# Kernel optimization log

Hardware: AMD Instinct MI355X
Metric: run time of the kernel (lower is better)

## Reference

```python
import jax, jax.numpy as jnp
import numpy as np

N, D0, D1, D2 = 8192, 512, 256, 64


def setup_inputs() -> dict:
    key = jax.random.key(0)
    k1, k2, k3, k4 = jax.random.split(key, 4)
    xi = jax.random.normal(k1, (N, D0), dtype=jnp.float32)
    # graph filter ~ row-normalized adjacency: nonnegative, entries O(1/N)
    filter_matrix = jax.random.uniform(k2, (N, N), dtype=jnp.float32) * (2.0 / N)
    b1 = np.sqrt(6.0 / (D0 + D1))
    b2 = np.sqrt(6.0 / (D1 + D2))
    w1 = jax.random.uniform(k3, (D0, D1), dtype=jnp.float32, minval=-b1, maxval=b1)
    w2 = jax.random.uniform(k4, (D1, D2), dtype=jnp.float32, minval=-b2, maxval=b2)
    return {"xi": xi, "filter_matrix": filter_matrix, "w1": w1, "w2": w2}


def reference(xi, filter_matrix, w1, w2):
    # two GCN layers: F @ (X @ W)
    h = jax.nn.relu(filter_matrix @ (xi @ w1))          # [N, D1]
    emb = filter_matrix @ (h @ w2)                       # [N, D2]
    # pairwise squared Euclidean distances between rows of emb -> [N, N]
    sq = jnp.sum(emb * emb, axis=1)                      # [N]
    dists = jnp.maximum(sq[:, None] + sq[None, :] - 2.0 * (emb @ emb.T), 0.0)
    recons_w = jax.nn.softmax(-dists, axis=1)            # row softmax of negative distances
    return emb, recons_w + 1e-10
```

## Files before the change

kernel.cpp:

```cpp
#include <hip/hip_runtime.h>

typedef short s16x8 __attribute__((ext_vector_type(8)));
typedef float f32x4 __attribute__((ext_vector_type(4)));
typedef unsigned int u32;

#define DEV static __device__ __forceinline__

DEV unsigned short f2bf(float x){
  u32 u = __builtin_bit_cast(u32, x);
  return (unsigned short)((u + 0x7FFFu + ((u >> 16) & 1u)) >> 16);
}
DEV float bf2f(unsigned short h){ u32 u = ((u32)h) << 16; return __builtin_bit_cast(float, u); }
DEV u32 pack2(float a, float b){ return (u32)f2bf(a) | ((u32)f2bf(b) << 16); }

DEV void gld16(const void* g, void* l){
  __builtin_amdgcn_global_load_lds((const __attribute__((address_space(1))) u32*)g,
                                   (__attribute__((address_space(3))) u32*)l, 16, 0, 0);
}

__global__ void k_cvt(const float* __restrict__ src, unsigned short* __restrict__ dst, long n4){
  long i = (long)blockIdx.x*256 + threadIdx.x;
  long stride = (long)gridDim.x*256;
  for (; i < n4; i += stride){
    float4 v = ((const float4*)src)[i];
    int2 p; p.x = (int)pack2(v.x, v.y); p.y = (int)pack2(v.z, v.w);
    ((int2*)dst)[i] = p;
  }
}

__global__ void k_transpose_bf16(const float* __restrict__ src,
                                 unsigned short* __restrict__ dst, int R, int C){
  int idx = blockIdx.x * 256 + threadIdx.x;
  if (idx >= R * C) return;
  int r = idx / C, c = idx % C;
  dst[(size_t)c * R + r] = f2bf(src[idx]);
}

__global__ void k_relu_bf16(const float* __restrict__ src, unsigned short* __restrict__ dst, int n4){
  int idx = blockIdx.x*256 + threadIdx.x;
  if (idx >= n4) return;
  float4 v = ((const float4*)src)[idx];
  int2 p;
  p.x = (int)pack2(fmaxf(v.x,0.f), fmaxf(v.y,0.f));
  p.y = (int)pack2(fmaxf(v.z,0.f), fmaxf(v.w,0.f));
  ((int2*)dst)[idx] = p;
}

template<int ROWS,int BK,int THREADS>
DEV void stage_lds(const unsigned short* __restrict__ src, int row0, int ld,
                   int kk, char* lds, int tid){
  constexpr int SLOTS = BK/8, SLM = SLOTS-1, RPC = 64/SLOTS;
  constexpr int NCH = ROWS*BK*2/1024;
  constexpr int NW = THREADS/64, NI = NCH/NW;
  static_assert(NI*NW==NCH, "chunk exact");
  const int lane = tid & 63, wid = tid >> 6;
  #pragma unroll
  for (int i=0;i<NI;i++){
    int c = i*NW + wid;
    int r = c*RPC + lane/SLOTS;
    int s = lane & SLM;
    int ks = s ^ (r & SLM);
    gld16(src + (size_t)(row0+r)*ld + kk + ks*8, lds + c*1024);
  }
}

template<int BM,int BN,int BK,int WR,int WC,bool ATOMIC>
__global__ __launch_bounds__(WR*WC*64)
void k_gemm(const unsigned short* __restrict__ A, const unsigned short* __restrict__ B,
            void* __restrict__ Cp, int lda, int ldb, int ldc, int kchunk)
{
  constexpr int THREADS = WR*WC*64;
  constexpr int ROWB = BK*2, SLM = BK/8 - 1;
  constexpr int ABYTES = BM*ROWB, BBYTES = BN*ROWB;
  constexpr int WM = BM/WR, WN = BN/WC;
  constexpr int FM = WM/16, FN = WN/16, KS = BK/32;

  __shared__ char smem[2*(ABYTES+BBYTES)];
  char* A0 = smem; char* B0 = A0 + ABYTES;
  char* A1 = B0 + BBYTES; char* B1 = A1 + ABYTES;

  const int tid = threadIdx.x, lane = tid & 63;
  const int wid = tid >> 6, wrr = wid / WC, wcc = wid % WC;
  const int m0 = blockIdx.y * BM, n0 = blockIdx.x * BN;
  const int kbeg = blockIdx.z * kchunk, nk = kchunk / BK;

  f32x4 acc[FM][FN];
  f32x4 z4 = {0.f,0.f,0.f,0.f};
  #pragma unroll
  for (int m=0;m<FM;m++)
    #pragma unroll
    for (int n=0;n<FN;n++) acc[m][n] = z4;

  auto issue = [&](int kk, char* bA, char* bB){
    stage_lds<BM,BK,THREADS>(A, m0, lda, kk, bA, tid);
    stage_lds<BN,BK,THREADS>(B, n0, ldb, kk, bB, tid);
  };
  auto compute = [&](const char* bA, const char* bB){
    #pragma unroll
    for (int ks=0;ks<KS;ks++){
      s16x8 av[FM], bv[FN];
      #pragma unroll
      for (int m=0;m<FM;m++){
        int r = wrr*WM + m*16 + (lane&15);
        int s = (ks*4 + (lane>>4)) ^ (r & SLM);
        av[m] = *(const s16x8*)(bA + r*ROWB + s*16);
      }
      #pragma unroll
      for (int n=0;n<FN;n++){
        int r = wcc*WN + n*16 + (lane&15);
        int s = (ks*4 + (lane>>4)) ^ (r & SLM);
        bv[n] = *(const s16x8*)(bB + r*ROWB + s*16);
      }
      #pragma unroll
      for (int m=0;m<FM;m++)
        #pragma unroll
        for (int n=0;n<FN;n++)
          acc[m][n] = __builtin_amdgcn_mfma_f32_16x16x32_bf16(av[m], bv[n], acc[m][n], 0, 0, 0);
    }
  };

  issue(kbeg, A0, B0);
  __syncthreads();

  for (int t=0;t<nk;t++){
    char* cA = (t&1)?A1:A0; char* cB = (t&1)?B1:B0;
    char* nA = (t&1)?A0:A1; char* nB = (t&1)?B0:B1;
    if (t+1 < nk) issue(kbeg + (t+1)*BK, nA, nB);
    compute(cA, cB);
    __syncthreads();
  }

  if constexpr (ATOMIC) {
    float* Cf = (float*)Cp;
    #pragma unroll
    for (int m=0;m<FM;m++)
      #pragma unroll
      for (int n=0;n<FN;n++)
        #pragma unroll
        for (int r=0;r<4;r++){
          int row = m0 + wrr*WM + m*16 + (lane>>4)*4 + r;
          int col = n0 + wcc*WN + n*16 + (lane&15);
          atomicAdd(Cf + (size_t)row*ldc + col, acc[m][n][r]);
        }
  } else {
    unsigned short* Ch = (unsigned short*)Cp;
    #pragma unroll
    for (int m=0;m<FM;m++)
      #pragma unroll
      for (int n=0;n<FN;n++)
        #pragma unroll
        for (int r=0;r<4;r++){
          int row = m0 + wrr*WM + m*16 + (lane>>4)*4 + r;
          int col = n0 + wcc*WN + n*16 + (lane&15);
          Ch[(size_t)row*ldc + col] = f2bf(acc[m][n][r]);
        }
  }
}

__global__ void k_emb_fin(const float* __restrict__ acc, float* __restrict__ emb_out,
                          unsigned short* __restrict__ embb, float* __restrict__ sq){
  int idx = blockIdx.x*256 + threadIdx.x;
  float v = acc[idx];
  emb_out[idx] = v;
  unsigned short ub = f2bf(v);
  embb[idx] = ub;
  float x = bf2f(ub);
  float s = x*x;
  #pragma unroll
  for (int off=32; off>0; off>>=1) s += __shfl_xor(s, off, 64);
  if ((threadIdx.x & 63)==0) sq[idx>>6] = s;
}

template<int PASS>
__global__ __launch_bounds__(256)
void k_dist(const unsigned short* __restrict__ embb, const float* __restrict__ sq,
            float* __restrict__ S, float* __restrict__ out)
{
  constexpr int ROWB = 128, SLM = 7;
  __shared__ char smem[2*128*128];
  char* bufA = smem;
  char* bufB = smem + 128*ROWB;
  const int tid=threadIdx.x, lane=tid&63, wid=tid>>6;
  const int wrr = wid>>1, wcc = wid&1;
  const int i0 = blockIdx.y*128, j0 = blockIdx.x*128;

  #pragma unroll
  for (int i=0;i<4;i++){
    int u = tid + i*256;
    int r = u>>3, c = u&7;
    int byte = r*ROWB + ((c^(r&SLM))*16);
    *(int4*)(bufA+byte) = *(const int4*)(embb + (size_t)(i0+r)*64 + c*8);
    *(int4*)(bufB+byte) = *(const int4*)(embb + (size_t)(j0+r)*64 + c*8);
  }
  __syncthreads();

  f32x4 acc[4][4];
  f32x4 z4 = {0.f,0.f,0.f,0.f};
  #pragma unroll
  for (int m=0;m<4;m++)
    #pragma unroll
    for (int n=0;n<4;n++) acc[m][n]=z4;

  #pragma unroll
  for (int ks=0;ks<2;ks++){
    s16x8 av[4], bv[4];
    #pragma unroll
    for (int m=0;m<4;m++){
      int r = wrr*64 + m*16 + (lane&15);
      int slot = (ks*4 + (lane>>4)) ^ (r&SLM);
      av[m] = *(const s16x8*)(bufA + r*ROWB + slot*16);
    }
    #pragma unroll
    for (int n=0;n<4;n++){
      int r = wcc*64 + n*16 + (lane&15);
      int slot = (ks*4 + (lane>>4)) ^ (r&SLM);
      bv[n] = *(const s16x8*)(bufB + r*ROWB + slot*16);
    }
    #pragma unroll
    for (int m=0;m<4;m++)
      #pragma unroll
      for (int n=0;n<4;n++)
        acc[m][n] = __builtin_amdgcn_mfma_f32_16x16x32_bf16(av[m], bv[n], acc[m][n], 0, 0, 0);
  }

  float sqj[4];
  #pragma unroll
  for (int n=0;n<4;n++) sqj[n] = sq[j0 + wcc*64 + n*16 + (lane&15)];

  #pragma unroll
  for (int m=0;m<4;m++){
    #pragma unroll
    for (int r=0;r<4;r++){
      int row = i0 + wrr*64 + m*16 + (lane>>4)*4 + r;
      float sqi = sq[row];
      if constexpr (PASS==1){
        float v = 0.f;
        #pragma unroll
        for (int n=0;n<4;n++){
          float d = fmaxf(sqi + sqj[n] - 2.f*acc[m][n][r], 0.f);
          v += __expf(-d);
        }
        #pragma unroll
        for (int off=1; off<16; off<<=1) v += __shfl_xor(v, off, 64);
        if ((lane&15)==0) atomicAdd(S+row, v);
      } else {
        float inv = 1.0f / S[row];
        #pragma unroll
        for (int n=0;n<4;n++){
          int col = j0 + wcc*64 + n*16 + (lane&15);
          float d = fmaxf(sqi + sqj[n] - 2.f*acc[m][n][r], 0.f);
          out[(size_t)row*8192 + col] = __expf(-d)*inv + 1e-10f;
        }
      }
    }
  }
}

extern "C" void kernel_launch(void* const* d_in, const int* in_sizes, int n_in,
                              void* d_out, int out_size, void* d_ws, size_t ws_size,
                              hipStream_t stream)
{
  const float* xi = (const float*)d_in[0];
  const float* F  = (const float*)d_in[1];
  const float* w1 = (const float*)d_in[2];
  const float* w2 = (const float*)d_in[3];
  float* out = (float*)d_out;
  float* emb_out = out;
  float* recons  = out + (size_t)8192*64;

  unsigned short* Fb = (unsigned short*)recons;

  char* ws = (char*)d_ws;
  size_t off = 0;
  auto alloc = [&](size_t bytes)->char*{ char* p = ws + off; off += (bytes + 255) & ~(size_t)255; return p; };
  unsigned short* w1t  = (unsigned short*)alloc((size_t)256*512*2);
  unsigned short* w2t  = (unsigned short*)alloc((size_t)64*256*2);
  unsigned short* xib  = (unsigned short*)alloc((size_t)8192*512*2);
  unsigned short* t1t  = (unsigned short*)alloc((size_t)256*8192*2);
  unsigned short* t2t  = (unsigned short*)alloc((size_t)64*8192*2);
  unsigned short* h    = (unsigned short*)alloc((size_t)8192*256*2);
  unsigned short* embb = (unsigned short*)alloc((size_t)8192*64*2);
  float* sq    = (float*)alloc((size_t)8192*4);
  char* zbase = ws + off;
  float* h_acc   = (float*)alloc((size_t)8192*256*4);
  float* emb_acc = (float*)alloc((size_t)8192*64*4);
  float* S       = (float*)alloc((size_t)8192*4);
  size_t zbytes = (size_t)((ws + off) - zbase);

  hipMemsetAsync(zbase, 0, zbytes, stream);

  k_cvt<<<dim3(2048),256,0,stream>>>(F,  Fb,  (long)8192*8192/4);
  k_cvt<<<dim3(2048),256,0,stream>>>(xi, xib, (long)8192*512/4);
  k_transpose_bf16<<<dim3((512*256+255)/256), 256, 0, stream>>>(w1, w1t, 512, 256);
  k_transpose_bf16<<<dim3((256*64+255)/256),  256, 0, stream>>>(w2, w2t, 256, 64);

  k_gemm<128,64,64,2,2,false><<<dim3(128,2,1),256,0,stream>>>(
      w1t, xib, t1t, 512, 512, 8192, 512);

  k_gemm<128,256,32,2,4,true><<<dim3(1,64,8),512,0,stream>>>(
      Fb, t1t, h_acc, 8192, 8192, 256, 1024);

  k_relu_bf16<<<dim3(8192*256/4/256),256,0,stream>>>(h_acc, h, 8192*256/4);

  k_gemm<64,64,64,2,2,false><<<dim3(128,1,1),256,0,stream>>>(
      w2t, h, t2t, 256, 256, 8192, 256);

  k_gemm<128,64,64,2,2,true><<<dim3(1,64,8),256,0,stream>>>(
      Fb, t2t, emb_acc, 8192, 8192, 64, 1024);

  k_emb_fin<<<dim3(8192*64/256),256,0,stream>>>(emb_acc, emb_out, embb, sq);

  k_dist<1><<<dim3(64,64),256,0,stream>>>(embb, sq, S, recons);
  k_dist<2><<<dim3(64,64),256,0,stream>>>(embb, sq, S, recons);
}
```

Baseline: 360.5 us.

## Triple-buffer GEMM LDS staging with explicit vmcnt waits

Replaces the double-buffered LDS pipeline with three stages, prefetching two K-tiles ahead. Explicit s_waitcnt vmcnt waits let the current tile's loads complete while the next tile's loads stay in flight, and sched barriers bracket the workgroup barriers. The aim is to hide more global-load latency behind MFMA compute. The cost is 1.5x the LDS footprint, which may reduce occupancy, and correctness now depends on the hand-computed per-thread load count L.

```diff
diff --git a/kernel.cpp b/kernel.cpp
--- a/kernel.cpp
+++ b/kernel.cpp
@@ -16,6 +16,24 @@
 DEV void gld16(const void* g, void* l){
   __builtin_amdgcn_global_load_lds((const __attribute__((address_space(1))) u32*)g,
                                    (__attribute__((address_space(3))) u32*)l, 16, 0, 0);
+}
+
+template<int N> DEV void vmwait(){
+  static_assert(N>=0 && N<=8, "vmcnt range");
+  if constexpr (N==0) asm volatile("s_waitcnt vmcnt(0)" ::: "memory");
+  else if constexpr (N==1) asm volatile("s_waitcnt vmcnt(1)" ::: "memory");
+  else if constexpr (N==2) asm volatile("s_waitcnt vmcnt(2)" ::: "memory");
+  else if constexpr (N==3) asm volatile("s_waitcnt vmcnt(3)" ::: "memory");
+  else if constexpr (N==4) asm volatile("s_waitcnt vmcnt(4)" ::: "memory");
+  else if constexpr (N==5) asm volatile("s_waitcnt vmcnt(5)" ::: "memory");
+  else if constexpr (N==6) asm volatile("s_waitcnt vmcnt(6)" ::: "memory");
+  else if constexpr (N==7) asm volatile("s_waitcnt vmcnt(7)" ::: "memory");
+  else                     asm volatile("s_waitcnt vmcnt(8)" ::: "memory");
+}
+DEV void pipebar(){
+  __builtin_amdgcn_sched_barrier(0);
+  __builtin_amdgcn_s_barrier();
+  __builtin_amdgcn_sched_barrier(0);
 }
 
 __global__ void k_cvt(const float* __restrict__ src, unsigned short* __restrict__ dst, long n4){
@@ -71,13 +89,14 @@
 {
   constexpr int THREADS = WR*WC*64;
   constexpr int ROWB = BK*2, SLM = BK/8 - 1;
-  constexpr int ABYTES = BM*ROWB, BBYTES = BN*ROWB;
+  constexpr int TBYTES = (BM+BN)*ROWB;
   constexpr int WM = BM/WR, WN = BN/WC;
   constexpr int FM = WM/16, FN = WN/16, KS = BK/32;
-
-  __shared__ char smem[2*(ABYTES+BBYTES)];
-  char* A0 = smem; char* B0 = A0 + ABYTES;
-  char* A1 = B0 + BBYTES; char* B1 = A1 + ABYTES;
+  constexpr int LA = BM*BK*2/1024/(THREADS/64);
+  constexpr int LB = BN*BK*2/1024/(THREADS/64);
+  constexpr int L  = LA + LB;
+
+  __shared__ char smem[3*TBYTES];
 
   const int tid = threadIdx.x, lane = tid & 63;
   const int wid = tid >> 6, wrr = wid / WC, wcc = wid % WC;
@@ -91,11 +110,13 @@
     #pragma unroll
     for (int n=0;n<FN;n++) acc[m][n] = z4;
 
-  auto issue = [&](int kk, char* bA, char* bB){
-    stage_lds<BM,BK,THREADS>(A, m0, lda, kk, bA, tid);
-    stage_lds<BN,BK,THREADS>(B, n0, ldb, kk, bB, tid);
+  auto stage = [&](int kk, char* b){
+    stage_lds<BM,BK,THREADS>(A, m0, lda, kk, b, tid);
+    stage_lds<BN,BK,THREADS>(B, n0, ldb, kk, b + BM*ROWB, tid);
   };
-  auto compute = [&](const char* bA, const char* bB){
+  auto compute = [&](const char* b){
+    const char* bA = b;
+    const char* bB = b + BM*ROWB;
     #pragma unroll
     for (int ks=0;ks<KS;ks++){
       s16x8 av[FM], bv[FN];
@@ -119,15 +140,21 @@
     }
   };
 
-  issue(kbeg, A0, B0);
-  __syncthreads();
-
-  for (int t=0;t<nk;t++){
-    char* cA = (t&1)?A1:A0; char* cB = (t&1)?B1:B0;
-    char* nA = (t&1)?A0:A1; char* nB = (t&1)?B0:B1;
-    if (t+1 < nk) issue(kbeg + (t+1)*BK, nA, nB);
-    compute(cA, cB);
-    __syncthreads();
+  char* bc = smem;
+  char* b1 = smem + TBYTES;
+  char* b2 = smem + 2*TBYTES;
+
+  stage(kbeg, bc);
+  stage(kbeg + BK, b1);
+
+  for (int t=0; t<nk; t++){
+    if (t+1 < nk) vmwait<L>();
+    else          vmwait<0>();
+    pipebar();
+    if (t+2 < nk) stage(kbeg + (t+2)*BK, b2);
+    compute(bc);
+    pipebar();
+    char* tmp = bc; bc = b1; b1 = b2; b2 = tmp;
   }
 
   if constexpr (ATOMIC) {
```

New measurement: 351.2 us. 1.03x faster.
